# Kernel optimization log

Hardware: AMD Instinct MI355X
Metric: run time of the kernel (lower is better)

Reference implementation:

```python
import jax, jax.numpy as jnp
import numpy as np


def setup_inputs() -> dict:
    key = jax.random.key(0)
    k1, k2 = jax.random.split(key)
    B, DIM, T, SIZE = 64, 512, 2048, 1024
    H = jax.random.normal(k1, (B, DIM, T), dtype=jnp.float32)
    units = jax.random.normal(k2, (DIM, SIZE), dtype=jnp.float32)
    return {"H": H, "units": units}


def reference(H, units):
    # H: (B, dim, T), units: (dim, size)
    # Original: C[b, s, t] = exp(-||H[b,:,t] - units[:,s]||^2) normalized over s.
    # exp(-d^2) / sum_s exp(-d^2) == softmax(-d^2, axis=s).
    Ht = jnp.swapaxes(H, 1, 2)                      # (B, T, dim)
    h_sq = jnp.sum(Ht * Ht, axis=-1, keepdims=True)  # (B, T, 1)
    m_sq = jnp.sum(units * units, axis=0)            # (size,)
    cross = jnp.einsum('btd,ds->bts', Ht, units)     # (B, T, size) GEMM
    sqdist = h_sq - 2.0 * cross + m_sq               # (B, T, size)
    C = jax.nn.softmax(-sqdist, axis=-1)             # normalize over codebook
    return jnp.swapaxes(C, 1, 2)                     # (B, size, T)
```

## Files before the change

### kernel.cpp

```cpp
#include <hip/hip_runtime.h>
#include <stdint.h>


typedef unsigned short u16;
typedef __attribute__((ext_vector_type(8))) short short8;
typedef __attribute__((ext_vector_type(4))) float f32x4;
typedef __attribute__((ext_vector_type(16))) float f32x16;

#define B_DIM 64
#define DIM   512
#define T_DIM 2048
#define S_DIM 1024

#define ASLOT0 0
#define ASLOT1 65536
#define A_LO   32768
#define BRING  131072
#define MSQ_O  147456
#define REDM_O 151552
#define REDS_O 153600
#define SM_SZ  155648

__device__ __forceinline__ u16 f32_to_bf16(float f) {
  uint32_t u = __float_as_uint(f);
  uint32_t r = u + 0x7FFFu + ((u >> 16) & 1u);
  return (u16)(r >> 16);
}
__device__ __forceinline__ float bf16_to_f32(u16 h) {
  return __uint_as_float(((uint32_t)h) << 16);
}


__global__ __launch_bounds__(256) void k_prep_units(const float* __restrict__ units,
                                                    u16* __restrict__ UpH, u16* __restrict__ UpL,
                                                    float* __restrict__ msq) {
  const int s0 = blockIdx.x * 4;
  const int tid = threadIdx.x;
  const int lane = tid & 63, wv = tid >> 6;
  float acc0 = 0.f, acc1 = 0.f, acc2 = 0.f, acc3 = 0.f;
#pragma unroll
  for (int j = 0; j < 2; ++j) {
    const int d = tid + j * 256;
    const float4 v = *(const float4*)(units + (size_t)d * S_DIM + s0);
    acc0 += v.x * v.x; acc1 += v.y * v.y; acc2 += v.z * v.z; acc3 += v.w * v.w;
    const int dbase = (d >> 4) * 16384 + ((d >> 3) & 1) * 256 + (d & 7);
    const float fv[4] = {v.x, v.y, v.z, v.w};
#pragma unroll
    for (int q = 0; q < 4; ++q) {
      const int s = s0 + q;
      const int idx = dbase + ((s >> 5) * 64 + (s & 31)) * 8;
      const u16 h = f32_to_bf16(fv[q]);
      UpH[idx] = h;
      UpL[idx] = f32_to_bf16(fv[q] - bf16_to_f32(h));
    }
  }
#pragma unroll
  for (int off = 1; off < 64; off <<= 1) {
    acc0 += __shfl_xor(acc0, off);
    acc1 += __shfl_xor(acc1, off);
    acc2 += __shfl_xor(acc2, off);
    acc3 += __shfl_xor(acc3, off);
  }
  __shared__ float part[4][4];
  if (lane == 0) { part[wv][0] = acc0; part[wv][1] = acc1; part[wv][2] = acc2; part[wv][3] = acc3; }
  __syncthreads();
  if (tid < 4) msq[s0 + tid] = part[0][tid] + part[1][tid] + part[2][tid] + part[3][tid];
}

__global__ __launch_bounds__(256) void k_prep_h(const float* __restrict__ H,
                                                u16* __restrict__ BpH, u16* __restrict__ BpL) {
  __shared__ float tile[64 * 68];
  const int bx = blockIdx.x;
  const int d0 = blockIdx.y * 64;
  const int b = blockIdx.z;
  const int t0 = bx * 64;
  const int tid = threadIdx.x;
#pragma unroll
  for (int j = 0; j < 4; ++j) {
    const int chunk = tid + j * 256;
    const int r = chunk >> 4, c4 = (chunk & 15) * 4;
    const float4 v = *(const float4*)(H + ((size_t)(b * DIM + d0 + r)) * T_DIM + t0 + c4);
    *(float4*)(&tile[r * 68 + c4]) = v;
  }
  __syncthreads();
#pragma unroll
  for (int j = 0; j < 2; ++j) {
    const int chunk = tid + j * 256;
    const int q = chunk >> 3, e8 = (chunk & 7) * 8;
    union { u16 us[8]; uint4 v4; } hi, lo;
#pragma unroll
    for (int k = 0; k < 8; ++k) {
      const float f = tile[(e8 + k) * 68 + q];
      const u16 h = f32_to_bf16(f);
      hi.us[k] = h;
      lo.us[k] = f32_to_bf16(f - bf16_to_f32(h));
    }
    const int dg = d0 + e8;
    const int chunkB = (q >> 5) * 64 + ((dg >> 3) & 1) * 32 + (q & 31);
    const size_t o = ((((size_t)b * 32 + bx) * 32 + (dg >> 4)) * 128 + chunkB) * 8;
    *(uint4*)(BpH + o) = hi.v4;
    *(uint4*)(BpL + o) = lo.v4;
  }
}

__device__ __forceinline__ void gl16(const void* g, void* l) {
  __builtin_amdgcn_global_load_lds((const __attribute__((address_space(1))) void*)g,
                                   (__attribute__((address_space(3))) void*)l, 16, 0, 0);
}

#define WAITV(N) asm volatile("s_waitcnt vmcnt(" #N ")" ::: "memory")
#define SYNCPT() do { __builtin_amdgcn_s_barrier(); __builtin_amdgcn_sched_barrier(0); } while (0)

__global__ __launch_bounds__(512, 2) void k_fused(const u16* __restrict__ UpH, const u16* __restrict__ UpL,
                                                  const u16* __restrict__ BpH, const u16* __restrict__ BpL,
                                                  const float* __restrict__ msq,
                                                  float* __restrict__ out) {
  __shared__ __align__(16) char sm[SM_SZ];
  const int tid = threadIdx.x;
  const int lane = tid & 63, wv = tid >> 6;
  const int l31 = lane & 31, lhi = lane >> 5;
  const int sw = wv;
  const int g = wv & 3;

  const int tgx = blockIdx.x;
  const int t00 = tgx * 64;
  const int bb = blockIdx.y;

  const char* const upH = (const char*)UpH + (size_t)(sw * 256 + lane) * 16;
  const char* const upL = (const char*)UpL + (size_t)(sw * 256 + lane) * 16;
  const char* const bp = ((g < 2) ? (const char*)BpH : (const char*)BpL)
                         + (((size_t)bb * 32 + tgx) * 32) * 2048
                         + (size_t)((g & 1) * 64 + lane) * 16;
  const int dA = (sw * 256 + lane) * 16;
  const int dB = BRING + ((g < 2) ? 0 : 2048) + ((g & 1) * 64 + lane) * 16;

#define ST_AH(SL, KS, I) gl16(upH + (size_t)(KS) * 32768 + (I) * 1024, sm + (SL) + (I) * 1024 + dA)
#define ST_AL(SL, KS, I) gl16(upL + (size_t)(KS) * 32768 + (I) * 1024, sm + (SL) + A_LO + (I) * 1024 + dA)
#define ST_B(KS)         gl16(bp + (size_t)(KS) * 2048, sm + (((KS) & 3) * 4096) + dB)

  const int offA = sw * 4096 + lane * 16;
  const int offB = lane * 16;

  f32x16 acc[4][2];
#pragma unroll
  for (int mt = 0; mt < 4; ++mt)
#pragma unroll
    for (int nt = 0; nt < 2; ++nt)
#pragma unroll
      for (int r = 0; r < 16; ++r)
        acc[mt][nt][r] = 0.f;

  gl16((const char*)msq + g * 1024 + lane * 16, sm + MSQ_O + g * 1024 + lane * 16);
  ST_B(0);
  ST_AH(ASLOT0, 0, 0); ST_AH(ASLOT0, 0, 1); ST_AH(ASLOT0, 0, 2); ST_AH(ASLOT0, 0, 3);
  ST_AL(ASLOT0, 0, 0); ST_AL(ASLOT0, 0, 1); ST_AL(ASLOT0, 0, 2); ST_AL(ASLOT0, 0, 3);
  ST_B(1);

#pragma unroll 1
  for (int k = 0; k < 32; ++k) {
    const int cur = (k & 1) << 16;
    const int nxt = 65536 - cur;
    const int ksA = (k + 1 < 32) ? (k + 1) : 31;
    const int ksB = (k + 2 < 32) ? (k + 2) : 31;
    const int rb = BRING + (k & 3) * 4096;

    WAITV(4);
    SYNCPT();

    short8 ah[4], al[4], bh[2], bl[2];
#pragma unroll
    for (int mt = 0; mt < 4; ++mt) ah[mt] = *(const short8*)(sm + cur + offA + mt * 1024);
    bh[0] = *(const short8*)(sm + rb + offB);
    bh[1] = *(const short8*)(sm + rb + 1024 + offB);
    ST_B(ksB);
    ST_AH(nxt, ksA, 0); ST_AH(nxt, ksA, 1);
    __builtin_amdgcn_s_setprio(1);
#pragma unroll
    for (int mt = 0; mt < 4; ++mt) {
      acc[mt][0] = __builtin_amdgcn_mfma_f32_32x32x16_bf16(ah[mt], bh[0], acc[mt][0], 0, 0, 0);
      acc[mt][1] = __builtin_amdgcn_mfma_f32_32x32x16_bf16(ah[mt], bh[1], acc[mt][1], 0, 0, 0);
    }
    __builtin_amdgcn_s_setprio(0);
    bl[0] = *(const short8*)(sm + rb + 2048 + offB);
    bl[1] = *(const short8*)(sm + rb + 3072 + offB);
    ST_AH(nxt, ksA, 2); ST_AH(nxt, ksA, 3);
    __builtin_amdgcn_s_setprio(1);
#pragma unroll
    for (int mt = 0; mt < 4; ++mt) {
      acc[mt][0] = __builtin_amdgcn_mfma_f32_32x32x16_bf16(ah[mt], bl[0], acc[mt][0], 0, 0, 0);
      acc[mt][1] = __builtin_amdgcn_mfma_f32_32x32x16_bf16(ah[mt], bl[1], acc[mt][1], 0, 0, 0);
    }
    __builtin_amdgcn_s_setprio(0);
    WAITV(5);
#pragma unroll
    for (int mt = 0; mt < 4; ++mt) al[mt] = *(const short8*)(sm + cur + A_LO + offA + mt * 1024);
    ST_AL(nxt, ksA, 0); ST_AL(nxt, ksA, 1); ST_AL(nxt, ksA, 2); ST_AL(nxt, ksA, 3);
    __builtin_amdgcn_s_setprio(1);
#pragma unroll
    for (int mt = 0; mt < 4; ++mt) {
      acc[mt][0] = __builtin_amdgcn_mfma_f32_32x32x16_bf16(al[mt], bh[0], acc[mt][0], 0, 0, 0);
      acc[mt][1] = __builtin_amdgcn_mfma_f32_32x32x16_bf16(al[mt], bh[1], acc[mt][1], 0, 0, 0);
    }
    __builtin_amdgcn_s_setprio(0);
  }

  const float* msql = (const float*)(sm + MSQ_O);
  float* redM = (float*)(sm + REDM_O);
  float* redS = (float*)(sm + REDS_O);

  float mx0 = -3.0e38f, mx1 = -3.0e38f;
#pragma unroll
  for (int mt = 0; mt < 4; ++mt) {
    const int sb = sw * 128 + mt * 32 + lhi * 4;
#pragma unroll
    for (int q = 0; q < 4; ++q) {
      const f32x4 mq = *(const f32x4*)(msql + sb + q * 8);
#pragma unroll
      for (int r = 0; r < 4; ++r) {
        const int reg = q * 4 + r;
        const float v0 = 2.f * acc[mt][0][reg] - mq[r];
        const float v1 = 2.f * acc[mt][1][reg] - mq[r];
        acc[mt][0][reg] = v0; acc[mt][1][reg] = v1;
        mx0 = fmaxf(mx0, v0); mx1 = fmaxf(mx1, v1);
      }
    }
  }
  mx0 = fmaxf(mx0, __shfl_xor(mx0, 32));
  mx1 = fmaxf(mx1, __shfl_xor(mx1, 32));
  if (lane < 32) { redM[wv * 64 + l31] = mx0; redM[wv * 64 + 32 + l31] = mx1; }
  __syncthreads();
  float M0 = redM[l31], M1 = redM[32 + l31];
#pragma unroll
  for (int w = 1; w < 8; ++w) {
    M0 = fmaxf(M0, redM[w * 64 + l31]);
    M1 = fmaxf(M1, redM[w * 64 + 32 + l31]);
  }
  float s0 = 0.f, s1 = 0.f;
#pragma unroll
  for (int mt = 0; mt < 4; ++mt)
#pragma unroll
    for (int reg = 0; reg < 16; ++reg) {
      const float e0 = __expf(acc[mt][0][reg] - M0);
      const float e1 = __expf(acc[mt][1][reg] - M1);
      acc[mt][0][reg] = e0; acc[mt][1][reg] = e1;
      s0 += e0; s1 += e1;
    }
  s0 += __shfl_xor(s0, 32);
  s1 += __shfl_xor(s1, 32);
  if (lane < 32) { redS[wv * 64 + l31] = s0; redS[wv * 64 + 32 + l31] = s1; }
  __syncthreads();
  float S0 = redS[l31], S1 = redS[32 + l31];
#pragma unroll
  for (int w = 1; w < 8; ++w) {
    S0 += redS[w * 64 + l31];
    S1 += redS[w * 64 + 32 + l31];
  }
  const float r0 = 1.0f / S0, r1 = 1.0f / S1;

  float* const outb = out + ((size_t)bb << 21);
  const int tc0 = t00 + l31, tc1 = t00 + 32 + l31;
#pragma unroll
  for (int mt = 0; mt < 4; ++mt) {
    const int sb = sw * 128 + mt * 32 + lhi * 4;
#pragma unroll
    for (int q = 0; q < 4; ++q)
#pragma unroll
      for (int r = 0; r < 4; ++r) {
        const int srow = sb + q * 8 + r;
        const int reg = q * 4 + r;
        outb[(size_t)srow * T_DIM + tc0] = acc[mt][0][reg] * r0;
        outb[(size_t)srow * T_DIM + tc1] = acc[mt][1][reg] * r1;
      }
  }
}

extern "C" void kernel_launch(void* const* d_in, const int* in_sizes, int n_in,
                              void* d_out, int out_size, void* d_ws, size_t ws_size,
                              hipStream_t stream) {
  (void)in_sizes; (void)n_in; (void)out_size; (void)ws_size;
  const float* H = (const float*)d_in[0];
  const float* units = (const float*)d_in[1];
  float* out = (float*)d_out;
  char* ws = (char*)d_ws;
  u16* BpH = (u16*)(ws);
  u16* BpL = (u16*)(ws + 134217728);
  u16* UpH = (u16*)(ws + 268435456);
  u16* UpL = (u16*)(ws + 269484032);
  float* msq = (float*)(ws + 270532608);

  k_prep_units<<<dim3(S_DIM / 4), 256, 0, stream>>>(units, UpH, UpL, msq);
  k_prep_h<<<dim3(T_DIM / 64, DIM / 64, B_DIM), 256, 0, stream>>>(H, BpH, BpL);
  k_fused<<<dim3(T_DIM / 64, B_DIM), 512, 0, stream>>>(UpH, UpL, BpH, BpL, msq, out);
}
```

Baseline: 592.6 us.

## Load GEMM fragments directly from global into registers, dropping LDS staging

```diff
diff --git a/kernel.cpp b/kernel.cpp
--- a/kernel.cpp
+++ b/kernel.cpp
@@ -12,15 +12,6 @@
 #define T_DIM 2048
 #define S_DIM 1024
 
-#define ASLOT0 0
-#define ASLOT1 65536
-#define A_LO   32768
-#define BRING  131072
-#define MSQ_O  147456
-#define REDM_O 151552
-#define REDS_O 153600
-#define SM_SZ  155648
-
 __device__ __forceinline__ u16 f32_to_bf16(float f) {
   uint32_t u = __float_as_uint(f);
   uint32_t r = u + 0x7FFFu + ((u >> 16) & 1u);
@@ -29,7 +20,6 @@
 __device__ __forceinline__ float bf16_to_f32(u16 h) {
   return __uint_as_float(((uint32_t)h) << 16);
 }
-
 
 __global__ __launch_bounds__(256) void k_prep_units(const float* __restrict__ units,
                                                     u16* __restrict__ UpH, u16* __restrict__ UpL,
@@ -103,43 +93,26 @@
   }
 }
 
-__device__ __forceinline__ void gl16(const void* g, void* l) {
-  __builtin_amdgcn_global_load_lds((const __attribute__((address_space(1))) void*)g,
-                                   (__attribute__((address_space(3))) void*)l, 16, 0, 0);
-}
-
-#define WAITV(N) asm volatile("s_waitcnt vmcnt(" #N ")" ::: "memory")
-#define SYNCPT() do { __builtin_amdgcn_s_barrier(); __builtin_amdgcn_sched_barrier(0); } while (0)
-
 __global__ __launch_bounds__(512, 2) void k_fused(const u16* __restrict__ UpH, const u16* __restrict__ UpL,
                                                   const u16* __restrict__ BpH, const u16* __restrict__ BpL,
                                                   const float* __restrict__ msq,
                                                   float* __restrict__ out) {
-  __shared__ __align__(16) char sm[SM_SZ];
+  __shared__ float redM[8][64];
+  __shared__ float redS[8][64];
   const int tid = threadIdx.x;
   const int lane = tid & 63, wv = tid >> 6;
   const int l31 = lane & 31, lhi = lane >> 5;
   const int sw = wv;
-  const int g = wv & 3;
 
   const int tgx = blockIdx.x;
   const int t00 = tgx * 64;
   const int bb = blockIdx.y;
 
-  const char* const upH = (const char*)UpH + (size_t)(sw * 256 + lane) * 16;
-  const char* const upL = (const char*)UpL + (size_t)(sw * 256 + lane) * 16;
-  const char* const bp = ((g < 2) ? (const char*)BpH : (const char*)BpL)
-                         + (((size_t)bb * 32 + tgx) * 32) * 2048
-                         + (size_t)((g & 1) * 64 + lane) * 16;
-  const int dA = (sw * 256 + lane) * 16;
-  const int dB = BRING + ((g < 2) ? 0 : 2048) + ((g & 1) * 64 + lane) * 16;
-
-#define ST_AH(SL, KS, I) gl16(upH + (size_t)(KS) * 32768 + (I) * 1024, sm + (SL) + (I) * 1024 + dA)
-#define ST_AL(SL, KS, I) gl16(upL + (size_t)(KS) * 32768 + (I) * 1024, sm + (SL) + A_LO + (I) * 1024 + dA)
-#define ST_B(KS)         gl16(bp + (size_t)(KS) * 2048, sm + (((KS) & 3) * 4096) + dB)
-
-  const int offA = sw * 4096 + lane * 16;
-  const int offB = lane * 16;
+  const char* const aH = (const char*)UpH + (sw * 4) * 1024 + lane * 16;
+  const char* const aL = (const char*)UpL + (sw * 4) * 1024 + lane * 16;
+  const size_t bg = (((size_t)bb * 32 + tgx) * 32) * 2048 + lane * 16;
+  const char* const bH = (const char*)BpH + bg;
+  const char* const bL = (const char*)BpL + bg;
 
   f32x16 acc[4][2];
 #pragma unroll
@@ -150,63 +123,57 @@
       for (int r = 0; r < 16; ++r)
         acc[mt][nt][r] = 0.f;
 
-  gl16((const char*)msq + g * 1024 + lane * 16, sm + MSQ_O + g * 1024 + lane * 16);
-  ST_B(0);
-  ST_AH(ASLOT0, 0, 0); ST_AH(ASLOT0, 0, 1); ST_AH(ASLOT0, 0, 2); ST_AH(ASLOT0, 0, 3);
-  ST_AL(ASLOT0, 0, 0); ST_AL(ASLOT0, 0, 1); ST_AL(ASLOT0, 0, 2); ST_AL(ASLOT0, 0, 3);
-  ST_B(1);
+  short8 ahA[4], ahB[4];
+  short8 bhA[2], bhB[2];
+  short8 al[4];
+  short8 bl[2];
+
+#define LD_AH(D, KS) do { const size_t ko = (size_t)(KS) * 32768;            \
+    (D)[0] = *(const short8*)(aH + ko);                                      \
+    (D)[1] = *(const short8*)(aH + ko + 1024);                               \
+    (D)[2] = *(const short8*)(aH + ko + 2048);                               \
+    (D)[3] = *(const short8*)(aH + ko + 3072); } while (0)
+#define LD_AL(D, KS) do { const size_t ko = (size_t)(KS) * 32768;            \
+    (D)[0] = *(const short8*)(aL + ko);                                      \
+    (D)[1] = *(const short8*)(aL + ko + 1024);                               \
+    (D)[2] = *(const short8*)(aL + ko + 2048);                               \
+    (D)[3] = *(const short8*)(aL + ko + 3072); } while (0)
+#define LD_BH(D, KS) do { const size_t ko = (size_t)(KS) * 2048;             \
+    (D)[0] = *(const short8*)(bH + ko);                                      \
+    (D)[1] = *(const short8*)(bH + ko + 1024); } while (0)
+#define LD_BL(D, KS) do { const size_t ko = (size_t)(KS) * 2048;             \
+    (D)[0] = *(const short8*)(bL + ko);                                      \
+    (D)[1] = *(const short8*)(bL + ko + 1024); } while (0)
+
+#define MM8(AF, BF)                                                          \
+    __builtin_amdgcn_s_setprio(1);                                           \
+    _Pragma("unroll") for (int mt = 0; mt < 4; ++mt)                         \
+      _Pragma("unroll") for (int nt = 0; nt < 2; ++nt)                       \
+        acc[mt][nt] = __builtin_amdgcn_mfma_f32_32x32x16_bf16((AF)[mt], (BF)[nt], acc[mt][nt], 0, 0, 0); \
+    __builtin_amdgcn_s_setprio(0);
+
+  LD_AH(ahA, 0); LD_BH(bhA, 0); LD_BL(bl, 0); LD_AL(al, 0);
+  LD_AH(ahB, 1); LD_BH(bhB, 1);
 
 #pragma unroll 1
-  for (int k = 0; k < 32; ++k) {
-    const int cur = (k & 1) << 16;
-    const int nxt = 65536 - cur;
-    const int ksA = (k + 1 < 32) ? (k + 1) : 31;
-    const int ksB = (k + 2 < 32) ? (k + 2) : 31;
-    const int rb = BRING + (k & 3) * 4096;
-
-    WAITV(4);
-    SYNCPT();
-
-    short8 ah[4], al[4], bh[2], bl[2];
-#pragma unroll
-    for (int mt = 0; mt < 4; ++mt) ah[mt] = *(const short8*)(sm + cur + offA + mt * 1024);
-    bh[0] = *(const short8*)(sm + rb + offB);
-    bh[1] = *(const short8*)(sm + rb + 1024 + offB);
-    ST_B(ksB);
-    ST_AH(nxt, ksA, 0); ST_AH(nxt, ksA, 1);
-    __builtin_amdgcn_s_setprio(1);
-#pragma unroll
-    for (int mt = 0; mt < 4; ++mt) {
-      acc[mt][0] = __builtin_amdgcn_mfma_f32_32x32x16_bf16(ah[mt], bh[0], acc[mt][0], 0, 0, 0);
-      acc[mt][1] = __builtin_amdgcn_mfma_f32_32x32x16_bf16(ah[mt], bh[1], acc[mt][1], 0, 0, 0);
-    }
-    __builtin_amdgcn_s_setprio(0);
-    bl[0] = *(const short8*)(sm + rb + 2048 + offB);
-    bl[1] = *(const short8*)(sm + rb + 3072 + offB);
-    ST_AH(nxt, ksA, 2); ST_AH(nxt, ksA, 3);
-    __builtin_amdgcn_s_setprio(1);
-#pragma unroll
-    for (int mt = 0; mt < 4; ++mt) {
-      acc[mt][0] = __builtin_amdgcn_mfma_f32_32x32x16_bf16(ah[mt], bl[0], acc[mt][0], 0, 0, 0);
-      acc[mt][1] = __builtin_amdgcn_mfma_f32_32x32x16_bf16(ah[mt], bl[1], acc[mt][1], 0, 0, 0);
-    }
-    __builtin_amdgcn_s_setprio(0);
-    WAITV(5);
-#pragma unroll
-    for (int mt = 0; mt < 4; ++mt) al[mt] = *(const short8*)(sm + cur + A_LO + offA + mt * 1024);
-    ST_AL(nxt, ksA, 0); ST_AL(nxt, ksA, 1); ST_AL(nxt, ksA, 2); ST_AL(nxt, ksA, 3);
-    __builtin_amdgcn_s_setprio(1);
-#pragma unroll
-    for (int mt = 0; mt < 4; ++mt) {
-      acc[mt][0] = __builtin_amdgcn_mfma_f32_32x32x16_bf16(al[mt], bh[0], acc[mt][0], 0, 0, 0);
-      acc[mt][1] = __builtin_amdgcn_mfma_f32_32x32x16_bf16(al[mt], bh[1], acc[mt][1], 0, 0, 0);
-    }
-    __builtin_amdgcn_s_setprio(0);
-  }
-
-  const float* msql = (const float*)(sm + MSQ_O);
-  float* redM = (float*)(sm + REDM_O);
-  float* redS = (float*)(sm + REDS_O);
+  for (int k = 0; k < 32; k += 2) {
+    const int kc2 = (k + 2 < 32) ? (k + 2) : 30;
+    const int kc3 = (k + 3 < 32) ? (k + 3) : 31;
+    MM8(ahA, bhA);
+    MM8(ahA, bl);
+    LD_BL(bl, k + 1);
+    LD_AH(ahA, kc2);
+    MM8(al, bhA);
+    LD_AL(al, k + 1);
+    LD_BH(bhA, kc2);
+    MM8(ahB, bhB);
+    MM8(ahB, bl);
+    LD_BL(bl, kc2);
+    LD_AH(ahB, kc3);
+    MM8(al, bhB);
+    LD_AL(al, kc2);
+    LD_BH(bhB, kc3);
+  }
 
   float mx0 = -3.0e38f, mx1 = -3.0e38f;
 #pragma unroll
@@ -214,7 +181,7 @@
     const int sb = sw * 128 + mt * 32 + lhi * 4;
 #pragma unroll
     for (int q = 0; q < 4; ++q) {
-      const f32x4 mq = *(const f32x4*)(msql + sb + q * 8);
+      const f32x4 mq = *(const f32x4*)(msq + sb + q * 8);
 #pragma unroll
       for (int r = 0; r < 4; ++r) {
         const int reg = q * 4 + r;
@@ -227,13 +194,13 @@
   }
   mx0 = fmaxf(mx0, __shfl_xor(mx0, 32));
   mx1 = fmaxf(mx1, __shfl_xor(mx1, 32));
-  if (lane < 32) { redM[wv * 64 + l31] = mx0; redM[wv * 64 + 32 + l31] = mx1; }
-  __syncthreads();
-  float M0 = redM[l31], M1 = redM[32 + l31];
+  if (lane < 32) { redM[wv][l31] = mx0; redM[wv][32 + l31] = mx1; }
+  __syncthreads();
+  float M0 = redM[0][l31], M1 = redM[0][32 + l31];
 #pragma unroll
   for (int w = 1; w < 8; ++w) {
-    M0 = fmaxf(M0, redM[w * 64 + l31]);
-    M1 = fmaxf(M1, redM[w * 64 + 32 + l31]);
+    M0 = fmaxf(M0, redM[w][l31]);
+    M1 = fmaxf(M1, redM[w][32 + l31]);
   }
   float s0 = 0.f, s1 = 0.f;
 #pragma unroll
@@ -247,13 +214,13 @@
     }
   s0 += __shfl_xor(s0, 32);
   s1 += __shfl_xor(s1, 32);
-  if (lane < 32) { redS[wv * 64 + l31] = s0; redS[wv * 64 + 32 + l31] = s1; }
-  __syncthreads();
-  float S0 = redS[l31], S1 = redS[32 + l31];
+  if (lane < 32) { redS[wv][l31] = s0; redS[wv][32 + l31] = s1; }
+  __syncthreads();
+  float S0 = redS[0][l31], S1 = redS[0][32 + l31];
 #pragma unroll
   for (int w = 1; w < 8; ++w) {
-    S0 += redS[w * 64 + l31];
-    S1 += redS[w * 64 + 32 + l31];
+    S0 += redS[w][l31];
+    S1 += redS[w][32 + l31];
   }
   const float r0 = 1.0f / S0, r1 = 1.0f / S1;
 
```

Result: faster. 572.3 us (-3.4%).
